# Kernel tuning notes

Hardware: AMD Instinct MI355X
Metric: run time of the kernel (lower is better)

Reference implementation:

```python
import jax, jax.numpy as jnp
import numpy as np

N_NODES = 100000
N_EDGES = 1600000
IN_DIM = 128
HID = 128
HEADS = 4
HEAD_DIM = HID // HEADS
OUT_DIM = 3
N_GRAPHS = 1024
BN_EPS = 1e-5


def setup_inputs() -> dict:
    key = jax.random.key(0)
    ks = jax.random.split(key, 32)
    inp = {}
    inp['x'] = jax.random.normal(ks[0], (N_NODES, IN_DIM), dtype=jnp.float32)
    inp['edge_index'] = jax.random.randint(ks[1], (2, N_EDGES), 0, N_NODES, dtype=jnp.int64)
    inp['edge_attr'] = jax.random.normal(ks[2], (N_EDGES,), dtype=jnp.float32)
    inp['batch'] = jnp.sort(jax.random.randint(ks[3], (N_NODES,), 0, N_GRAPHS, dtype=jnp.int64))
    s = 0.05
    inp['gat_w'] = jax.random.normal(ks[4], (IN_DIM, HID), jnp.float32) * s
    inp['gat_att_src'] = jax.random.normal(ks[5], (HEADS, HEAD_DIM), jnp.float32) * s
    inp['gat_att_dst'] = jax.random.normal(ks[6], (HEADS, HEAD_DIM), jnp.float32) * s
    inp['gat_b'] = jnp.zeros((HID,), jnp.float32)
    for i, k in zip((1, 2, 3), (ks[7], ks[8], ks[9])):
        inp[f'gcn{i}_w'] = jax.random.normal(k, (HID, HID), jnp.float32) * s
        inp[f'gcn{i}_b'] = jnp.zeros((HID,), jnp.float32)
        inp[f'bn{i}_g'] = jnp.ones((HID,), jnp.float32)
        inp[f'bn{i}_b'] = jnp.zeros((HID,), jnp.float32)
        inp[f'bn{i}_m'] = jax.random.normal(jax.random.fold_in(key, 100 + i), (HID,), jnp.float32) * 0.01
        inp[f'bn{i}_v'] = jnp.ones((HID,), jnp.float32)
    inp['p1_w'] = jax.random.normal(ks[10], (HID, HID), jnp.float32) * s
    inp['p1_b'] = jnp.zeros((HID,), jnp.float32)
    inp['p2_w'] = jax.random.normal(ks[11], (HID, HID // 2), jnp.float32) * s
    inp['p2_b'] = jnp.zeros((HID // 2,), jnp.float32)
    inp['cls_w'] = jax.random.normal(ks[12], (HID // 2, OUT_DIM), jnp.float32) * s
    inp['cls_b'] = jnp.zeros((OUT_DIM,), jnp.float32)
    return inp


def _add_self_loops(edge_index, n):
    ar = jnp.arange(n, dtype=edge_index.dtype)
    return jnp.concatenate([edge_index, jnp.stack([ar, ar])], axis=1)


def _gat(x, ei, w, att_src, att_dst, bias):
    # PyG GATConv: per-head linear, additive attention, softmax over incoming edges.
    n = x.shape[0]
    h = (x @ w).reshape(n, HEADS, HEAD_DIM)
    a_src = jnp.einsum('nhd,hd->nh', h, att_src)  # [N,H]
    a_dst = jnp.einsum('nhd,hd->nh', h, att_dst)
    src, dst = ei[0], ei[1]
    e = jax.nn.leaky_relu(a_src[src] + a_dst[dst], 0.2)  # [E,H]
    m = jax.ops.segment_max(e, dst, num_segments=n)       # per-dst max
    e = jnp.exp(e - m[dst])
    denom = jax.ops.segment_sum(e, dst, num_segments=n)
    alpha = e / denom[dst]                                 # self-loops => denom > 0
    msg = h[src] * alpha[:, :, None]                       # [E,H,D]
    out = jax.ops.segment_sum(msg, dst, num_segments=n)
    return out.reshape(n, HID) + bias


def _gcn(x, ei, w, bias):
    # PyG GCNConv with symmetric normalization and self-loops (already added).
    n = x.shape[0]
    src, dst = ei[0], ei[1]
    deg = jax.ops.segment_sum(jnp.ones_like(dst, dtype=x.dtype), dst, num_segments=n)
    dinv = jnp.where(deg > 0, jax.lax.rsqrt(deg), 0.0)
    norm = dinv[src] * dinv[dst]                           # [E]
    xw = x @ w
    out = jax.ops.segment_sum(norm[:, None] * xw[src], dst, num_segments=n)
    return out + bias


def _bn(x, g, b, m, v):
    return (x - m) * jax.lax.rsqrt(v + BN_EPS) * g + b


def reference(x, edge_index, edge_attr, batch,
              gat_w, gat_att_src, gat_att_dst, gat_b,
              gcn1_w, gcn1_b, gcn2_w, gcn2_b, gcn3_w, gcn3_b,
              bn1_g, bn1_b, bn1_m, bn1_v,
              bn2_g, bn2_b, bn2_m, bn2_v,
              bn3_g, bn3_b, bn3_m, bn3_v,
              p1_w, p1_b, p2_w, p2_b, cls_w, cls_b):
    n = x.shape[0]
    ei = _add_self_loops(edge_index, n)
    # eval mode: dropout is identity, BN uses running stats
    h = jax.nn.elu(_gat(x, ei, gat_w, gat_att_src, gat_att_dst, gat_b))
    idn = h
    h = jax.nn.elu(_bn(_gcn(h, ei, gcn1_w, gcn1_b), bn1_g, bn1_b, bn1_m, bn1_v)) + idn
    idn = h
    h = jax.nn.elu(_bn(_gcn(h, ei, gcn2_w, gcn2_b), bn2_g, bn2_b, bn2_m, bn2_v)) + idn
    h = jax.nn.elu(_bn(_gcn(h, ei, gcn3_w, gcn3_b), bn3_g, bn3_b, bn3_m, bn3_v))
    # global mean pool over graphs
    sums = jax.ops.segment_sum(h, batch, num_segments=N_GRAPHS)
    cnts = jax.ops.segment_sum(jnp.ones((n,), h.dtype), batch, num_segments=N_GRAPHS)
    g = sums / jnp.maximum(cnts, 1.0)[:, None]
    emb = jax.nn.elu(g @ p1_w + p1_b)
    emb = emb @ p2_w + p2_b
    out = emb @ cls_w + cls_b
    return out, emb
```

## Files before the change

### kernel.cpp

```cpp
#include <hip/hip_runtime.h>
#include <math.h>

#define BN_EPS 1e-5f
typedef unsigned short u16;
typedef __attribute__((ext_vector_type(8))) short bf16x8;
typedef __attribute__((ext_vector_type(4))) float f32x4;

__device__ inline unsigned bfpack2(float a, float b){
  unsigned ua = __float_as_uint(a); ua = (ua + 0x7fffu + ((ua >> 16) & 1u)) >> 16;
  unsigned ub = __float_as_uint(b); ub = (ub + 0x7fffu + ((ub >> 16) & 1u)) >> 16;
  return ua | (ub << 16);
}
__device__ inline u16 bf16of(float a){
  unsigned ua = __float_as_uint(a); return (u16)((ua + 0x7fffu + ((ua >> 16) & 1u)) >> 16);
}
__device__ inline float bflo(unsigned u){ return __uint_as_float(u << 16); }
__device__ inline float bfhi(unsigned u){ return __uint_as_float(u & 0xffff0000u); }

__global__ void k_count(const int* __restrict__ ei, int E, int N, int* __restrict__ deg){
  int chunk = blockIdx.x & 7;
  int e = (blockIdx.x >> 3)*256 + threadIdx.x;
  int ET = E + N;
  if (e >= ET) return;
  int csz = (N + 7) >> 3;
  int lo = chunk*csz, hi = lo + csz; if (hi > N) hi = N;
  int dst = (e < E) ? ei[E + e] : (e - E);
  if (dst < lo || dst >= hi) return;
  atomicAdd(&deg[dst], 1);
}

__global__ __launch_bounds__(1024) void k_scan_block(const int* __restrict__ deg, int* __restrict__ offs,
                                                     int* __restrict__ part, int N){
  __shared__ int sh[1024];
  int t = threadIdx.x; int i = blockIdx.x*1024 + t;
  int v = (i < N) ? ((deg[i] + 7) & ~7) : 0;
  sh[t] = v; __syncthreads();
  for (int off = 1; off < 1024; off <<= 1){
    int u = (t >= off) ? sh[t - off] : 0;
    __syncthreads();
    sh[t] += u;
    __syncthreads();
  }
  if (i < N) offs[i] = sh[t] - v;
  if (t == 1023) part[blockIdx.x] = sh[1023];
}

__global__ void k_scan_part(int* part, int nb){
  if (threadIdx.x == 0 && blockIdx.x == 0){
    int s = 0;
    for (int i = 0; i < nb; ++i){ int v = part[i]; part[i] = s; s += v; }
  }
}

__global__ void k_add_part(int* __restrict__ offs, const int* __restrict__ part,
                           const int* __restrict__ deg, int* __restrict__ csr, int N){
  int i = blockIdx.x*256 + threadIdx.x;
  if (i >= N) return;
  int o = offs[i] + part[i >> 10];
  offs[i] = o;
  int d = deg[i];
  int dp = (d + 7) & ~7;
  for (int j = d; j < dp; ++j) csr[o + j] = N;
}

__global__ void k_fill(const int* __restrict__ ei, int E, int N, const int* __restrict__ offs,
                       int* __restrict__ cursor, int* __restrict__ csr){
  int chunk = blockIdx.x & 7;
  int e = (blockIdx.x >> 3)*256 + threadIdx.x;
  int ET = E + N;
  if (e >= ET) return;
  int csz = (N + 7) >> 3;
  int lo = chunk*csz, hi = lo + csz; if (hi > N) hi = N;
  int src, dst;
  if (e < E){
    dst = ei[E + e];
    if (dst < lo || dst >= hi) return;
    src = ei[e];
  } else {
    src = e - E; dst = src;
    if (dst < lo || dst >= hi) return;
  }
  int pos = offs[dst] + atomicAdd(&cursor[dst], 1);
  csr[pos] = src;
}

__global__ void k_wconv4(const float* __restrict__ W0, const float* __restrict__ W1,
                         const float* __restrict__ W2, const float* __restrict__ W3,
                         u16* __restrict__ WbT){
  int gid = blockIdx.x*256 + threadIdx.x;
  int w = gid >> 14, id = gid & 16383;
  const float* W = (w == 0) ? W0 : (w == 1) ? W1 : (w == 2) ? W2 : W3;
  int nn = id >> 7, kk = id & 127;
  WbT[gid] = bf16of(W[kk*128 + nn]);
}

__global__ void k_bnfold(const float* b1, const float* g1, const float* bb1, const float* m1, const float* v1,
                         const float* b2, const float* g2, const float* bb2, const float* m2, const float* v2,
                         const float* b3, const float* g3, const float* bb3, const float* m3, const float* v3,
                         float* __restrict__ S, float* __restrict__ T){
  int t = threadIdx.x;
  int layer = t >> 7, c = t & 127;
  const float *gb, *g, *bb, *m, *v;
  if (layer == 0){ gb=b1; g=g1; bb=bb1; m=m1; v=v1; }
  else if (layer == 1){ gb=b2; g=g2; bb=bb2; m=m2; v=v2; }
  else { gb=b3; g=g3; bb=bb3; m=m3; v=v3; }
  float s = g[c] * rsqrtf(v[c] + BN_EPS);
  S[t] = s;
  T[t] = (gb[c] - m[c]) * s + bb[c];
}

__global__ __launch_bounds__(256) void k_gemm_mfma(const float* __restrict__ Af,
                                                   const u16* __restrict__ Ab,
                                                   const u16* __restrict__ WbT,
                                                   u16* __restrict__ Yb, int M,
                                                   const int* __restrict__ deg){
  int lane = threadIdx.x & 63;
  int wv   = threadIdx.x >> 6;
  int row0 = blockIdx.x * 128 + wv * 32;
  int l15  = lane & 15;
  int g    = lane >> 4;
  int rA0  = row0 + l15;       if (rA0 >= M) rA0 = M - 1;
  int rA1  = row0 + 16 + l15;  if (rA1 >= M) rA1 = M - 1;

  bf16x8 afr0[4], afr1[4];
  if (Ab){
    const u16* ap0 = Ab + (size_t)rA0*128 + g*8;
    const u16* ap1 = Ab + (size_t)rA1*128 + g*8;
    #pragma unroll
    for (int s = 0; s < 4; ++s){
      afr0[s] = *(const bf16x8*)(ap0 + s*32);
      afr1[s] = *(const bf16x8*)(ap1 + s*32);
    }
  } else {
    const float* ap0 = Af + (size_t)rA0*128 + g*8;
    const float* ap1 = Af + (size_t)rA1*128 + g*8;
    #pragma unroll
    for (int s = 0; s < 4; ++s){
      float4 f0 = *(const float4*)(ap0 + s*32);
      float4 f1 = *(const float4*)(ap0 + s*32 + 4);
      union { bf16x8 v; unsigned u[4]; } t0;
      t0.u[0] = bfpack2(f0.x, f0.y); t0.u[1] = bfpack2(f0.z, f0.w);
      t0.u[2] = bfpack2(f1.x, f1.y); t0.u[3] = bfpack2(f1.z, f1.w);
      afr0[s] = t0.v;
      float4 f2 = *(const float4*)(ap1 + s*32);
      float4 f3 = *(const float4*)(ap1 + s*32 + 4);
      union { bf16x8 v; unsigned u[4]; } t1;
      t1.u[0] = bfpack2(f2.x, f2.y); t1.u[1] = bfpack2(f2.z, f2.w);
      t1.u[2] = bfpack2(f3.x, f3.y); t1.u[3] = bfpack2(f3.z, f3.w);
      afr1[s] = t1.v;
    }
  }

  f32x4 acc0[8] = {}, acc1[8] = {};
  #pragma unroll
  for (int s = 0; s < 4; ++s){
    union BU { uint4 q; bf16x8 v; } b[8];
    #pragma unroll
    for (int t = 0; t < 8; ++t){
      int col = t*16 + l15;
      b[t].q = ((const uint4*)(WbT + (size_t)col*128))[s*4 + g];
    }
    #pragma unroll
    for (int t = 0; t < 8; ++t){
      acc0[t] = __builtin_amdgcn_mfma_f32_16x16x32_bf16(afr0[s], b[t].v, acc0[t], 0, 0, 0);
      acc1[t] = __builtin_amdgcn_mfma_f32_16x16x32_bf16(afr1[s], b[t].v, acc1[t], 0, 0, 0);
    }
  }

  #pragma unroll
  for (int j = 0; j < 4; ++j){
    int r0 = row0 + g*4 + j;
    if (r0 < M){
      float sc = deg ? rsqrtf((float)deg[r0]) : 1.0f;
      #pragma unroll
      for (int t = 0; t < 8; ++t)
        Yb[(size_t)r0*128 + t*16 + l15] = bf16of(acc0[t][j] * sc);
    }
    int r1 = row0 + 16 + g*4 + j;
    if (r1 < M){
      float sc = deg ? rsqrtf((float)deg[r1]) : 1.0f;
      #pragma unroll
      for (int t = 0; t < 8; ++t)
        Yb[(size_t)r1*128 + t*16 + l15] = bf16of(acc1[t][j] * sc);
    }
  }
}

__global__ __launch_bounds__(256) void k_attn(const unsigned* __restrict__ Yb, const float* __restrict__ asrcw,
                                              const float* __restrict__ adstw,
                                              float* __restrict__ a_src, float* __restrict__ a_dst, int N){
  if (blockIdx.x == 0 && threadIdx.x < 4) a_src[(size_t)N*4 + threadIdx.x] = -1e38f;
  int n = (blockIdx.x*256 + threadIdx.x) >> 6;
  int lane = threadIdx.x & 63;
  if (n >= N) return;
  int head = lane >> 4;
  int d0 = (lane & 15) * 2;
  unsigned u = Yb[(size_t)n*64 + lane];
  float h0 = bflo(u), h1 = bfhi(u);
  float vs = h0 * asrcw[head*32 + d0] + h1 * asrcw[head*32 + d0 + 1];
  float vd = h0 * adstw[head*32 + d0] + h1 * adstw[head*32 + d0 + 1];
  #pragma unroll
  for (int m = 1; m < 16; m <<= 1){
    vs += __shfl_xor(vs, m, 64);
    vd += __shfl_xor(vd, m, 64);
  }
  if ((lane & 15) == 0){
    a_src[n*4 + head] = vs;
    a_dst[n*4 + head] = vd;
  }
}

__global__ __launch_bounds__(256) void k_gat_agg(const uint4* __restrict__ Yb4, const int* __restrict__ csr,
                                                 const int* __restrict__ offs, const int* __restrict__ deg,
                                                 const float* __restrict__ asrc, const float* __restrict__ adst,
                                                 const float* __restrict__ bias, u16* __restrict__ outb, int N){
  int n = blockIdx.x*16 + (threadIdx.x >> 4);
  int l = threadIdx.x & 15;
  if (n >= N) return;
  int head = l >> 2;
  int beg = offs[n], d = deg[n];
  int dp = (d + 7) & ~7;
  const uint4* cp4 = (const uint4*)(csr + beg);
  float adh = adst[n*4 + head];
  float a[8] = {};
  float sw = 0.f;
  uint4 ia = cp4[0], ib = cp4[1];
  for (int i = 0; i < dp; i += 8){
    int nx = (i + 8 < dp) ? ((i + 8) >> 2) : 0;
    uint4 na = cp4[nx], nb = cp4[nx + 1];
    uint4 v0 = Yb4[(size_t)ia.x*16 + l];
    uint4 v1 = Yb4[(size_t)ia.y*16 + l];
    uint4 v2 = Yb4[(size_t)ia.z*16 + l];
    uint4 v3 = Yb4[(size_t)ia.w*16 + l];
    uint4 v4 = Yb4[(size_t)ib.x*16 + l];
    uint4 v5 = Yb4[(size_t)ib.y*16 + l];
    uint4 v6 = Yb4[(size_t)ib.z*16 + l];
    uint4 v7 = Yb4[(size_t)ib.w*16 + l];
    float e0 = asrc[(size_t)ia.x*4 + head];
    float e1 = asrc[(size_t)ia.y*4 + head];
    float e2 = asrc[(size_t)ia.z*4 + head];
    float e3 = asrc[(size_t)ia.w*4 + head];
    float e4 = asrc[(size_t)ib.x*4 + head];
    float e5 = asrc[(size_t)ib.y*4 + head];
    float e6 = asrc[(size_t)ib.z*4 + head];
    float e7 = asrc[(size_t)ib.w*4 + head];
    float w[8];
    float ee[8] = {e0,e1,e2,e3,e4,e5,e6,e7};
    #pragma unroll
    for (int j = 0; j < 8; ++j){
      float e = ee[j] + adh; e = e > 0.f ? e : 0.2f*e;
      w[j] = __expf(e);
      sw += w[j];
    }
    uint4 vv[8] = {v0,v1,v2,v3,v4,v5,v6,v7};
    #pragma unroll
    for (int j = 0; j < 8; ++j){
      unsigned u0 = vv[j].x, u1 = vv[j].y, u2 = vv[j].z, u3 = vv[j].w;
      float wj = w[j];
      a[0] += wj*bflo(u0); a[1] += wj*bfhi(u0);
      a[2] += wj*bflo(u1); a[3] += wj*bfhi(u1);
      a[4] += wj*bflo(u2); a[5] += wj*bfhi(u2);
      a[6] += wj*bflo(u3); a[7] += wj*bfhi(u3);
    }
    ia = na; ib = nb;
  }
  float inv = 1.f / sw;
  int c0 = l*8;
  float4 b0 = *(const float4*)(bias + c0);
  float4 b1 = *(const float4*)(bias + c0 + 4);
  float bb8[8] = {b0.x,b0.y,b0.z,b0.w,b1.x,b1.y,b1.z,b1.w};
  float og[8];
  #pragma unroll
  for (int c = 0; c < 8; ++c){
    float z = a[c]*inv + bb8[c];
    og[c] = z > 0.f ? z : expm1f(z);
  }
  uint4 o;
  o.x = bfpack2(og[0], og[1]);
  o.y = bfpack2(og[2], og[3]);
  o.z = bfpack2(og[4], og[5]);
  o.w = bfpack2(og[6], og[7]);
  ((uint4*)(outb + (size_t)n*128))[l] = o;
}

__global__ __launch_bounds__(256) void k_gcn_agg(const uint4* __restrict__ Yb4, const u16* __restrict__ residb,
                                                 u16* __restrict__ outb, float* __restrict__ outf,
                                                 const int* __restrict__ csr,
                                                 const int* __restrict__ offs, const int* __restrict__ deg,
                                                 const float* __restrict__ S, const float* __restrict__ T, int N){
  int n = blockIdx.x*16 + (threadIdx.x >> 4);
  int l = threadIdx.x & 15;
  if (n >= N) return;
  int beg = offs[n], d = deg[n];
  int dp = (d + 7) & ~7;
  const uint4* cp4 = (const uint4*)(csr + beg);
  float a[8] = {};
  uint4 ia = cp4[0], ib = cp4[1];
  for (int i = 0; i < dp; i += 8){
    int nx = (i + 8 < dp) ? ((i + 8) >> 2) : 0;
    uint4 na = cp4[nx], nb = cp4[nx + 1];
    uint4 v0 = Yb4[(size_t)ia.x*16 + l];
    uint4 v1 = Yb4[(size_t)ia.y*16 + l];
    uint4 v2 = Yb4[(size_t)ia.z*16 + l];
    uint4 v3 = Yb4[(size_t)ia.w*16 + l];
    uint4 v4 = Yb4[(size_t)ib.x*16 + l];
    uint4 v5 = Yb4[(size_t)ib.y*16 + l];
    uint4 v6 = Yb4[(size_t)ib.z*16 + l];
    uint4 v7 = Yb4[(size_t)ib.w*16 + l];
    uint4 vv[8] = {v0,v1,v2,v3,v4,v5,v6,v7};
    #pragma unroll
    for (int j = 0; j < 8; ++j){
      unsigned u0 = vv[j].x, u1 = vv[j].y, u2 = vv[j].z, u3 = vv[j].w;
      a[0] += bflo(u0); a[1] += bfhi(u0);
      a[2] += bflo(u1); a[3] += bfhi(u1);
      a[4] += bflo(u2); a[5] += bfhi(u2);
      a[6] += bflo(u3); a[7] += bfhi(u3);
    }
    ia = na; ib = nb;
  }
  float dinv = rsqrtf((float)d);
  int c0 = l*8;
  float4 S0 = *(const float4*)(S + c0), S1 = *(const float4*)(S + c0 + 4);
  float4 T0 = *(const float4*)(T + c0), T1 = *(const float4*)(T + c0 + 4);
  float ss[8] = {S0.x,S0.y,S0.z,S0.w,S1.x,S1.y,S1.z,S1.w};
  float tt[8] = {T0.x,T0.y,T0.z,T0.w,T1.x,T1.y,T1.z,T1.w};
  float rr[8] = {};
  if (residb){
    uint4 r = ((const uint4*)(residb + (size_t)n*128))[l];
    rr[0]=bflo(r.x); rr[1]=bfhi(r.x); rr[2]=bflo(r.y); rr[3]=bfhi(r.y);
    rr[4]=bflo(r.z); rr[5]=bfhi(r.z); rr[6]=bflo(r.w); rr[7]=bfhi(r.w);
  }
  float og[8];
  #pragma unroll
  for (int c = 0; c < 8; ++c){
    float z = a[c]*dinv*ss[c] + tt[c];
    z = z > 0.f ? z : expm1f(z);
    og[c] = z + rr[c];
  }
  if (outb){
    uint4 o;
    o.x = bfpack2(og[0], og[1]);
    o.y = bfpack2(og[2], og[3]);
    o.z = bfpack2(og[4], og[5]);
    o.w = bfpack2(og[6], og[7]);
    ((uint4*)(outb + (size_t)n*128))[l] = o;
  } else {
    float* op = outf + (size_t)n*128 + c0;
    *(float4*)op       = make_float4(og[0],og[1],og[2],og[3]);
    *(float4*)(op + 4) = make_float4(og[4],og[5],og[6],og[7]);
  }
}

__global__ __launch_bounds__(128) void k_pool(const float* __restrict__ H, const int* __restrict__ batch,
                                              float* __restrict__ G, int N){
  int gid = blockIdx.x; int c = threadIdx.x;
  int lo = 0, hi = N;
  while (lo < hi){ int mid = (lo + hi) >> 1; if (batch[mid] < gid) lo = mid + 1; else hi = mid; }
  int start = lo;
  lo = start; hi = N;
  while (lo < hi){ int mid = (lo + hi) >> 1; if (batch[mid] < gid + 1) lo = mid + 1; else hi = mid; }
  int end = lo;
  float acc = 0.f;
  for (int r = start; r < end; ++r) acc += H[(size_t)r*128 + c];
  float cnt = (float)(end - start);
  G[gid*128 + c] = acc / fmaxf(cnt, 1.0f);
}

__global__ __launch_bounds__(128) void k_mlp(const float* __restrict__ G, const float* __restrict__ p1w,
                                             const float* __restrict__ p1b, const float* __restrict__ p2w,
                                             const float* __restrict__ p2b, const float* __restrict__ cw,
                                             const float* __restrict__ cb, float* __restrict__ out, int NG){
  int gid = blockIdx.x; int t = threadIdx.x;
  __shared__ float gv[128], t1[128], e[64];
  gv[t] = G[gid*128 + t];
  __syncthreads();
  float acc = p1b[t];
  for (int k = 0; k < 128; ++k) acc += gv[k] * p1w[k*128 + t];
  t1[t] = acc > 0.f ? acc : expm1f(acc);
  __syncthreads();
  if (t < 64){
    float a = p2b[t];
    for (int k = 0; k < 128; ++k) a += t1[k] * p2w[k*64 + t];
    e[t] = a;
    out[NG*3 + gid*64 + t] = a;
  }
  __syncthreads();
  if (t < 3){
    float a = cb[t];
    for (int k = 0; k < 64; ++k) a += e[k] * cw[k*3 + t];
    out[gid*3 + t] = a;
  }
}

extern "C" void kernel_launch(void* const* d_in, const int* in_sizes, int n_in,
                              void* d_out, int out_size, void* d_ws, size_t ws_size,
                              hipStream_t stream){
  const float* x      = (const float*)d_in[0];
  const int*   ei     = (const int*)d_in[1];
  const int*   batch  = (const int*)d_in[3];
  const float* gat_w  = (const float*)d_in[4];
  const float* att_s  = (const float*)d_in[5];
  const float* att_d  = (const float*)d_in[6];
  const float* gat_b  = (const float*)d_in[7];
  const float* w1 = (const float*)d_in[8];  const float* b1 = (const float*)d_in[9];
  const float* bn1g = (const float*)d_in[10], *bn1b = (const float*)d_in[11],
             * bn1m = (const float*)d_in[12], *bn1v = (const float*)d_in[13];
  const float* w2 = (const float*)d_in[14]; const float* b2 = (const float*)d_in[15];
  const float* bn2g = (const float*)d_in[16], *bn2b = (const float*)d_in[17],
             * bn2m = (const float*)d_in[18], *bn2v = (const float*)d_in[19];
  const float* w3 = (const float*)d_in[20]; const float* b3 = (const float*)d_in[21];
  const float* bn3g = (const float*)d_in[22], *bn3b = (const float*)d_in[23],
             * bn3m = (const float*)d_in[24], *bn3v = (const float*)d_in[25];
  const float* p1w = (const float*)d_in[26]; const float* p1b = (const float*)d_in[27];
  const float* p2w = (const float*)d_in[28]; const float* p2b = (const float*)d_in[29];
  const float* cw  = (const float*)d_in[30]; const float* cb  = (const float*)d_in[31];

  int N  = in_sizes[3];
  int E  = in_sizes[1] / 2;
  int ET = E + N;
  int NG = out_size / 67;

  char* ws = (char*)d_ws;
  size_t off = 0;
  auto alloc = [&](size_t bytes) -> void* {
    void* p = ws + off;
    off = (off + bytes + 255) & ~(size_t)255;
    return p;
  };
  u16*      Abf  = (u16*)alloc((size_t)N * 128 * 2);
  u16*      Bbf  = (u16*)alloc((size_t)N * 128 * 2);
  float*    Bact = (float*)alloc((size_t)N * 128 * 4);
  u16*      Yb   = (u16*)alloc((size_t)(N + 1) * 128 * 2);
  int*      csr  = (int*)alloc((size_t)(ET + 7*N) * 4);
  int*      deg  = (int*)alloc((size_t)N * 4);
  int*      offs = (int*)alloc((size_t)N * 4);
  int*      curs = (int*)alloc((size_t)N * 4);
  int*      part = (int*)alloc(1024 * 4);
  float*    asrc = (float*)alloc((size_t)(N + 1) * 4 * 4);
  float*    adst = (float*)alloc((size_t)N * 4 * 4);
  float*    G    = (float*)alloc((size_t)NG * 128 * 4);
  u16*      Wb   = (u16*)alloc(65536 * 2);
  float*    bnS  = (float*)alloc(384 * 4);
  float*    bnT  = (float*)alloc(384 * 4);

  hipMemsetAsync(deg,  0, (size_t)N * 4, stream);
  hipMemsetAsync(curs, 0, (size_t)N * 4, stream);
  hipMemsetAsync(Yb + (size_t)N*128, 0, 256, stream);

  int nb = (N + 1023) / 1024;
  int bpp = (ET + 255)/256;
  k_count<<<8*bpp, 256, 0, stream>>>(ei, E, N, deg);
  k_scan_block<<<nb, 1024, 0, stream>>>(deg, offs, part, N);
  k_scan_part<<<1, 1, 0, stream>>>(part, nb);
  k_add_part<<<(N + 255)/256, 256, 0, stream>>>(offs, part, deg, csr, N);
  k_fill<<<8*bpp, 256, 0, stream>>>(ei, E, N, offs, curs, csr);

  k_wconv4<<<256, 256, 0, stream>>>(gat_w, w1, w2, w3, Wb);
  k_bnfold<<<1, 384, 0, stream>>>(b1, bn1g, bn1b, bn1m, bn1v,
                                  b2, bn2g, bn2b, bn2m, bn2v,
                                  b3, bn3g, bn3b, bn3m, bn3v, bnS, bnT);

  int gblk = (N + 127) / 128;
  int nblk16 = (N + 15) / 16;
  int ablk = (N + 3) / 4;

  k_gemm_mfma<<<gblk, 256, 0, stream>>>(x, nullptr, Wb, Yb, N, nullptr);
  k_attn<<<ablk, 256, 0, stream>>>((const unsigned*)Yb, att_s, att_d, asrc, adst, N);
  k_gat_agg<<<nblk16, 256, 0, stream>>>((const uint4*)Yb, csr, offs, deg, asrc, adst, gat_b, Abf, N);

  k_gemm_mfma<<<gblk, 256, 0, stream>>>(nullptr, Abf, Wb + 16384, Yb, N, deg);
  k_gcn_agg<<<nblk16, 256, 0, stream>>>((const uint4*)Yb, Abf, Bbf, nullptr, csr, offs, deg, bnS, bnT, N);
  k_gemm_mfma<<<gblk, 256, 0, stream>>>(nullptr, Bbf, Wb + 32768, Yb, N, deg);
  k_gcn_agg<<<nblk16, 256, 0, stream>>>((const uint4*)Yb, Bbf, Abf, nullptr, csr, offs, deg, bnS + 128, bnT + 128, N);
  k_gemm_mfma<<<gblk, 256, 0, stream>>>(nullptr, Abf, Wb + 49152, Yb, N, deg);
  k_gcn_agg<<<nblk16, 256, 0, stream>>>((const uint4*)Yb, nullptr, nullptr, Bact, csr, offs, deg, bnS + 256, bnT + 256, N);

  k_pool<<<NG, 128, 0, stream>>>(Bact, batch, G, N);
  k_mlp<<<NG, 128, 0, stream>>>(G, p1w, p1b, p2w, p2b, cw, cb, (float*)d_out, NG);
}
```

Baseline: 612.3 us.

## Bucket nodes by degree for balanced aggregation and reuse count ranks in CSR fill

Adds a degree histogram, bucket scan and permutation so the GAT and GCN aggregation kernels process nodes grouped by padded degree. This is meant to cut wavefront divergence, since each 16-lane group loops over its own neighbour count. It also records each edge's atomic rank during counting, so the CSR fill no longer needs a second atomic pass and the cursor memset goes away. The single-thread partial scan becomes a 1024-thread shuffle scan and the block scan uses wave shuffles. The cost is extra small kernels, a rank buffer sized by edge count, and output rows written in a scattered order.

New measurement: 1.329 ms. 117% more time.

```diff
diff --git a/kernel.cpp b/kernel.cpp
--- a/kernel.cpp
+++ b/kernel.cpp
@@ -2,6 +2,7 @@
 #include <math.h>
 
 #define BN_EPS 1e-5f
+#define NBUK 32
 typedef unsigned short u16;
 typedef __attribute__((ext_vector_type(8))) short bf16x8;
 typedef __attribute__((ext_vector_type(4))) float f32x4;
@@ -17,7 +18,8 @@
 __device__ inline float bflo(unsigned u){ return __uint_as_float(u << 16); }
 __device__ inline float bfhi(unsigned u){ return __uint_as_float(u & 0xffff0000u); }
 
-__global__ void k_count(const int* __restrict__ ei, int E, int N, int* __restrict__ deg){
+__global__ void k_count(const int* __restrict__ ei, int E, int N, int* __restrict__ deg,
+                        int* __restrict__ rank){
   int chunk = blockIdx.x & 7;
   int e = (blockIdx.x >> 3)*256 + threadIdx.x;
   int ET = E + N;
@@ -26,30 +28,63 @@
   int lo = chunk*csz, hi = lo + csz; if (hi > N) hi = N;
   int dst = (e < E) ? ei[E + e] : (e - E);
   if (dst < lo || dst >= hi) return;
-  atomicAdd(&deg[dst], 1);
+  rank[e] = atomicAdd(&deg[dst], 1);
 }
 
 __global__ __launch_bounds__(1024) void k_scan_block(const int* __restrict__ deg, int* __restrict__ offs,
                                                      int* __restrict__ part, int N){
-  __shared__ int sh[1024];
   int t = threadIdx.x; int i = blockIdx.x*1024 + t;
   int v = (i < N) ? ((deg[i] + 7) & ~7) : 0;
-  sh[t] = v; __syncthreads();
-  for (int off = 1; off < 1024; off <<= 1){
-    int u = (t >= off) ? sh[t - off] : 0;
-    __syncthreads();
-    sh[t] += u;
-    __syncthreads();
-  }
-  if (i < N) offs[i] = sh[t] - v;
-  if (t == 1023) part[blockIdx.x] = sh[1023];
-}
-
-__global__ void k_scan_part(int* part, int nb){
-  if (threadIdx.x == 0 && blockIdx.x == 0){
-    int s = 0;
-    for (int i = 0; i < nb; ++i){ int v = part[i]; part[i] = s; s += v; }
-  }
+  int lane = t & 63, wid = t >> 6;
+  int s = v;
+  #pragma unroll
+  for (int d = 1; d < 64; d <<= 1){
+    int u = __shfl_up(s, d, 64);
+    if (lane >= d) s += u;
+  }
+  __shared__ int wsum[16];
+  if (lane == 63) wsum[wid] = s;
+  __syncthreads();
+  if (t < 16){
+    int ws = wsum[t];
+    #pragma unroll
+    for (int d = 1; d < 16; d <<= 1){
+      int u = __shfl_up(ws, d, 16);
+      if (t >= d) ws += u;
+    }
+    wsum[t] = ws;
+  }
+  __syncthreads();
+  int base = (wid > 0) ? wsum[wid - 1] : 0;
+  if (i < N) offs[i] = base + s - v;
+  if (t == 1023) part[blockIdx.x] = base + s;
+}
+
+__global__ __launch_bounds__(1024) void k_scan_part(int* __restrict__ part, int nb){
+  int t = threadIdx.x;
+  int v = (t < nb) ? part[t] : 0;
+  int lane = t & 63, wid = t >> 6;
+  int s = v;
+  #pragma unroll
+  for (int d = 1; d < 64; d <<= 1){
+    int u = __shfl_up(s, d, 64);
+    if (lane >= d) s += u;
+  }
+  __shared__ int wsum[16];
+  if (lane == 63) wsum[wid] = s;
+  __syncthreads();
+  if (t < 16){
+    int ws = wsum[t];
+    #pragma unroll
+    for (int d = 1; d < 16; d <<= 1){
+      int u = __shfl_up(ws, d, 16);
+      if (t >= d) ws += u;
+    }
+    wsum[t] = ws;
+  }
+  __syncthreads();
+  int base = (wid > 0) ? wsum[wid - 1] : 0;
+  if (t < nb) part[t] = base + s - v;
 }
 
 __global__ void k_add_part(int* __restrict__ offs, const int* __restrict__ part,
@@ -64,7 +99,7 @@
 }
 
 __global__ void k_fill(const int* __restrict__ ei, int E, int N, const int* __restrict__ offs,
-                       int* __restrict__ cursor, int* __restrict__ csr){
+                       const int* __restrict__ rank, int* __restrict__ csr){
   int chunk = blockIdx.x & 7;
   int e = (blockIdx.x >> 3)*256 + threadIdx.x;
   int ET = E + N;
@@ -80,8 +115,45 @@
     src = e - E; dst = src;
     if (dst < lo || dst >= hi) return;
   }
-  int pos = offs[dst] + atomicAdd(&cursor[dst], 1);
-  csr[pos] = src;
+  csr[offs[dst] + rank[e]] = src;
+}
+
+__global__ void k_hist(const int* __restrict__ deg, int* __restrict__ bhist, int N){
+  __shared__ int h[NBUK];
+  if (threadIdx.x < NBUK) h[threadIdx.x] = 0;
+  __syncthreads();
+  int i = blockIdx.x*256 + threadIdx.x;
+  if (i < N){
+    int dp = (deg[i] + 7) >> 3;
+    int b = dp < NBUK ? dp : NBUK - 1;
+    atomicAdd(&h[b], 1);
+  }
+  __syncthreads();
+  if (threadIdx.x < NBUK && h[threadIdx.x]) atomicAdd(&bhist[threadIdx.x], h[threadIdx.x]);
+}
+
+__global__ void k_bucketscan(const int* __restrict__ bhist, int* __restrict__ boff,
+                             int* __restrict__ bcur){
+  int t = threadIdx.x;
+  int v = bhist[t];
+  int s = v;
+  #pragma unroll
+  for (int d = 1; d < 32; d <<= 1){
+    int u = __shfl_up(s, d, 32);
+    if (t >= d) s += u;
+  }
+  boff[t] = s - v;
+  bcur[t] = 0;
+}
+
+__global__ void k_permfill(const int* __restrict__ deg, const int* __restrict__ boff,
+                           int* __restrict__ bcur, int* __restrict__ perm, int N){
+  int i = blockIdx.x*256 + threadIdx.x;
+  if (i >= N) return;
+  int dp = (deg[i] + 7) >> 3;
+  int b = dp < NBUK ? dp : NBUK - 1;
+  int pos = atomicAdd(&bcur[b], 1);
+  perm[boff[b] + pos] = i;
 }
 
 __global__ void k_wconv4(const float* __restrict__ W0, const float* __restrict__ W1,
@@ -212,11 +284,13 @@
 
 __global__ __launch_bounds__(256) void k_gat_agg(const uint4* __restrict__ Yb4, const int* __restrict__ csr,
                                                  const int* __restrict__ offs, const int* __restrict__ deg,
+                                                 const int* __restrict__ perm,
                                                  const float* __restrict__ asrc, const float* __restrict__ adst,
                                                  const float* __restrict__ bias, u16* __restrict__ outb, int N){
-  int n = blockIdx.x*16 + (threadIdx.x >> 4);
+  int gid = blockIdx.x*16 + (threadIdx.x >> 4);
   int l = threadIdx.x & 15;
-  if (n >= N) return;
+  if (gid >= N) return;
+  int n = perm[gid];
   int head = l >> 2;
   int beg = offs[n], d = deg[n];
   int dp = (d + 7) & ~7;
@@ -287,10 +361,12 @@
                                                  u16* __restrict__ outb, float* __restrict__ outf,
                                                  const int* __restrict__ csr,
                                                  const int* __restrict__ offs, const int* __restrict__ deg,
+                                                 const int* __restrict__ perm,
                                                  const float* __restrict__ S, const float* __restrict__ T, int N){
-  int n = blockIdx.x*16 + (threadIdx.x >> 4);
+  int gid = blockIdx.x*16 + (threadIdx.x >> 4);
   int l = threadIdx.x & 15;
-  if (n >= N) return;
+  if (gid >= N) return;
+  int n = perm[gid];
   int beg = offs[n], d = deg[n];
   int dp = (d + 7) & ~7;
   const uint4* cp4 = (const uint4*)(csr + beg);
@@ -432,10 +508,14 @@
   float*    Bact = (float*)alloc((size_t)N * 128 * 4);
   u16*      Yb   = (u16*)alloc((size_t)(N + 1) * 128 * 2);
   int*      csr  = (int*)alloc((size_t)(ET + 7*N) * 4);
+  int*      rank = (int*)alloc((size_t)ET * 4);
   int*      deg  = (int*)alloc((size_t)N * 4);
   int*      offs = (int*)alloc((size_t)N * 4);
-  int*      curs = (int*)alloc((size_t)N * 4);
+  int*      perm = (int*)alloc((size_t)N * 4);
   int*      part = (int*)alloc(1024 * 4);
+  int*      bhist= (int*)alloc(NBUK * 4);
+  int*      boff = (int*)alloc(NBUK * 4);
+  int*      bcur = (int*)alloc(NBUK * 4);
   float*    asrc = (float*)alloc((size_t)(N + 1) * 4 * 4);
   float*    adst = (float*)alloc((size_t)N * 4 * 4);
   float*    G    = (float*)alloc((size_t)NG * 128 * 4);
@@ -444,16 +524,19 @@
   float*    bnT  = (float*)alloc(384 * 4);
 
   hipMemsetAsync(deg,  0, (size_t)N * 4, stream);
-  hipMemsetAsync(curs, 0, (size_t)N * 4, stream);
+  hipMemsetAsync(bhist, 0, NBUK * 4, stream);
   hipMemsetAsync(Yb + (size_t)N*128, 0, 256, stream);
 
   int nb = (N + 1023) / 1024;
   int bpp = (ET + 255)/256;
-  k_count<<<8*bpp, 256, 0, stream>>>(ei, E, N, deg);
+  k_count<<<8*bpp, 256, 0, stream>>>(ei, E, N, deg, rank);
   k_scan_block<<<nb, 1024, 0, stream>>>(deg, offs, part, N);
-  k_scan_part<<<1, 1, 0, stream>>>(part, nb);
+  k_scan_part<<<1, 1024, 0, stream>>>(part, nb);
+  k_hist<<<(N + 255)/256, 256, 0, stream>>>(deg, bhist, N);
+  k_bucketscan<<<1, NBUK, 0, stream>>>(bhist, boff, bcur);
   k_add_part<<<(N + 255)/256, 256, 0, stream>>>(offs, part, deg, csr, N);
-  k_fill<<<8*bpp, 256, 0, stream>>>(ei, E, N, offs, curs, csr);
+  k_permfill<<<(N + 255)/256, 256, 0, stream>>>(deg, boff, bcur, perm, N);
+  k_fill<<<8*bpp, 256, 0, stream>>>(ei, E, N, offs, rank, csr);
 
   k_wconv4<<<256, 256, 0, stream>>>(gat_w, w1, w2, w3, Wb);
   k_bnfold<<<1, 384, 0, stream>>>(b1, bn1g, bn1b, bn1m, bn1v,
@@ -466,14 +549,14 @@
 
   k_gemm_mfma<<<gblk, 256, 0, stream>>>(x, nullptr, Wb, Yb, N, nullptr);
   k_attn<<<ablk, 256, 0, stream>>>((const unsigned*)Yb, att_s, att_d, asrc, adst, N);
-  k_gat_agg<<<nblk16, 256, 0, stream>>>((const uint4*)Yb, csr, offs, deg, asrc, adst, gat_b, Abf, N);
+  k_gat_agg<<<nblk16, 256, 0, stream>>>((const uint4*)Yb, csr, offs, deg, perm, asrc, adst, gat_b, Abf, N);
 
   k_gemm_mfma<<<gblk, 256, 0, stream>>>(nullptr, Abf, Wb + 16384, Yb, N, deg);
-  k_gcn_agg<<<nblk16, 256, 0, stream>>>((const uint4*)Yb, Abf, Bbf, nullptr, csr, offs, deg, bnS, bnT, N);
+  k_gcn_agg<<<nblk16, 256, 0, stream>>>((const uint4*)Yb, Abf, Bbf, nullptr, csr, offs, deg, perm, bnS, bnT, N);
   k_gemm_mfma<<<gblk, 256, 0, stream>>>(nullptr, Bbf, Wb + 32768, Yb, N, deg);
-  k_gcn_agg<<<nblk16, 256, 0, stream>>>((const uint4*)Yb, Bbf, Abf, nullptr, csr, offs, deg, bnS + 128, bnT + 128, N);
+  k_gcn_agg<<<nblk16, 256, 0, stream>>>((const uint4*)Yb, Bbf, Abf, nullptr, csr, offs, deg, perm, bnS + 128, bnT + 128, N);
   k_gemm_mfma<<<gblk, 256, 0, stream>>>(nullptr, Abf, Wb + 49152, Yb, N, deg);
-  k_gcn_agg<<<nblk16, 256, 0, stream>>>((const uint4*)Yb, nullptr, nullptr, Bact, csr, offs, deg, bnS + 256, bnT + 256, N);
+  k_gcn_agg<<<nblk16, 256, 0, stream>>>((const uint4*)Yb, nullptr, nullptr, Bact, csr, offs, deg, perm, bnS + 256, bnT + 256, N);
 
   k_pool<<<NG, 128, 0, stream>>>(Bact, batch, G, N);
   k_mlp<<<NG, 128, 0, stream>>>(G, p1w, p1b, p2w, p2b, cw, cb, (float*)d_out, NG);
```
